# Kernel optimization log

Hardware: AMD Instinct MI355X
Metric: run time of the kernel (lower is better)

Reference implementation:

```python
import jax, jax.numpy as jnp
import numpy as np
import math

H = 128      # hidden_channels
R = 32       # num_rbf
N = 4096     # atoms
E = 65536    # edges
CU = 4.5     # cutoff_upper (cutoff_lower = 0)
ALPHA = 5.0 / CU
MEANS = jnp.linspace(math.exp(-CU), 1.0, R, dtype=jnp.float32)
BETA = jnp.float32((2.0 / R * (1.0 - math.exp(-CU))) ** -2)
EPS = 1e-5


def _ln(x, g, b):
    mu = x.mean(-1, keepdims=True)
    var = ((x - mu) ** 2).mean(-1, keepdims=True)
    return (x - mu) * jax.lax.rsqrt(var + EPS) * g + b


def setup_inputs() -> dict:
    key = jax.random.key(0)
    ks = jax.random.split(key, 20)
    f32 = jnp.float32

    def w(i, shape):
        return jax.random.normal(ks[i], shape, f32) / np.float32(np.sqrt(shape[-1]))

    return {
        "edge_vec": jax.random.normal(ks[0], (E, 3), f32) * 1.5,
        "emb_w": w(1, (128, H)),
        "emb2_w": w(2, (H, 2 * H)), "emb2_b": jnp.zeros((H,), f32),
        "dp1_w": w(3, (H, R)), "dp1_b": jnp.zeros((H,), f32),
        "dp2_w": w(4, (H, R)), "dp2_b": jnp.zeros((H,), f32),
        "dp3_w": w(5, (H, R)), "dp3_b": jnp.zeros((H,), f32),
        "lt0_w": w(6, (H, H)), "lt1_w": w(7, (H, H)), "lt2_w": w(8, (H, H)),
        "ls0_w": w(9, (2 * H, H)), "ls0_b": jnp.zeros((2 * H,), f32),
        "ls1_w": w(10, (3 * H, 2 * H)), "ls1_b": jnp.zeros((3 * H,), f32),
        "init_g": jnp.ones((H,), f32), "init_b": jnp.zeros((H,), f32),
        "lin_w": w(11, (H, 3 * H)), "lin_b": jnp.zeros((H,), f32),
        "outn_g": jnp.ones((3 * H,), f32), "outn_b": jnp.zeros((3 * H,), f32),
        "ol1_w": w(12, (H // 2, H)), "ol1_b": jnp.zeros((H // 2,), f32),
        "ol2_w": w(13, (1, H // 2)), "ol2_b": jnp.zeros((1,), f32),
        "z": jax.random.randint(ks[14], (N,), 0, 128, dtype=jnp.int32),
        "edge_index": jax.random.randint(ks[15], (2, E), 0, N, dtype=jnp.int32),
    }


def reference(edge_vec, emb_w, emb2_w, emb2_b, dp1_w, dp1_b, dp2_w, dp2_b,
              dp3_w, dp3_b, lt0_w, lt1_w, lt2_w, ls0_w, ls0_b, ls1_w, ls1_b,
              init_g, init_b, lin_w, lin_b, outn_g, outn_b, ol1_w, ol1_b,
              ol2_w, ol2_b, z, edge_index):
    n = z.shape[0]
    src, dst = edge_index[0], edge_index[1]

    d = jnp.sqrt((edge_vec ** 2).sum(-1))                 # (E,)
    vn = edge_vec / d[:, None]                             # unit edge vectors
    cut = jnp.where(d < CU, 0.5 * (jnp.cos(jnp.pi * d / CU) + 1.0), 0.0)
    # expnorm RBF
    rbf = cut[:, None] * jnp.exp(-BETA * (jnp.exp(-ALPHA * d)[:, None] - MEANS) ** 2)  # (E,R)

    # atomic-number message Zij = emb2(cat(emb(z_i), emb(z_j)))
    zpair = jnp.concatenate([emb_w[z[src]], emb_w[z[dst]]], -1)  # (E,2H)
    zij = zpair @ emb2_w.T + emb2_b                              # (E,H)
    c = cut[:, None] * zij                                       # cutoff * Zij, (E,H)

    w1 = (rbf @ dp1_w.T + dp1_b) * c    # scalar channel weights (E,H)
    w2 = (rbf @ dp2_w.T + dp2_b) * c
    w3 = (rbf @ dp3_w.T + dp3_b) * c

    eye = jnp.eye(3, dtype=edge_vec.dtype)
    zero = jnp.zeros_like(vn[:, 0])
    skew = jnp.stack([zero, -vn[:, 2], vn[:, 1],
                      vn[:, 2], zero, -vn[:, 0],
                      -vn[:, 1], vn[:, 0], zero], 1).reshape(-1, 3, 3)  # (E,3,3)
    outer = vn[:, :, None] * vn[:, None, :]
    sym = outer - ((vn ** 2).sum(-1) / 3.0)[:, None, None] * eye        # traceless sym (E,3,3)

    seg = lambda a: jax.ops.segment_sum(a, src, num_segments=n)
    I0 = seg(w1)[:, :, None, None] * eye                                # (N,H,3,3)
    A0 = seg(w2[:, :, None, None] * skew[:, None, :, :])                # (N,H,3,3)
    S0 = seg(w3[:, :, None, None] * sym[:, None, :, :])                 # (N,H,3,3)

    tn = ((I0 + A0 + S0) ** 2).sum((-2, -1))                            # tensor_norm, (N,H)
    nrm = _ln(tn, init_g, init_b)
    h = jax.nn.silu(nrm @ ls0_w.T + ls0_b)
    scal = jax.nn.silu(h @ ls1_w.T + ls1_b).reshape(n, H, 3)            # per-channel gates

    I1 = jnp.einsum('nhxy,gh->ngxy', I0, lt0_w) * scal[..., 0][..., None, None]
    A1 = jnp.einsum('nhxy,gh->ngxy', A0, lt1_w) * scal[..., 1][..., None, None]
    S1 = jnp.einsum('nhxy,gh->ngxy', S0, lt2_w) * scal[..., 2][..., None, None]

    x = jnp.concatenate([(I1 ** 2).sum((-2, -1)),
                         (A1 ** 2).sum((-2, -1)),
                         (S1 ** 2).sum((-2, -1))], -1)                  # (N,3H)
    x = _ln(x, outn_g, outn_b)
    s1 = x @ lin_w.T + lin_b
    s2 = jax.nn.silu(s1) @ ol1_w.T + ol1_b
    s3 = jax.nn.silu(s2) @ ol2_w.T + ol2_b                              # per-atom energy (N,1)
    return s3
```

## Files before the change

### kernel.cpp

```cpp
#include <hip/hip_runtime.h>
#include <math.h>

#define NH_TOT 524288
#define N_ATOM 4096
#define N_EDGE 65536

typedef __attribute__((ext_vector_type(8))) short bf16x8;
typedef __attribute__((ext_vector_type(4))) float f32x4;

__device__ __forceinline__ unsigned short f2bf(float f) {
    unsigned u = __builtin_bit_cast(unsigned, f);
    unsigned r = (u + 0x7fffu + ((u >> 16) & 1u)) >> 16;
    return (unsigned short)r;
}
__device__ __forceinline__ float silu(float v) { return v / (1.0f + __expf(-v)); }

#define WB_LS1 32768
#define WB_LT0 131072
#define WB_LT1 147456
#define WB_LT2 163840
#define WB_DP  180224

__global__ __launch_bounds__(256) void k_setup(
    const float* __restrict__ emb_w, const float* __restrict__ emb2_w,
    const int* __restrict__ ei,
    const float* __restrict__ ls0_w, const float* __restrict__ ls1_w,
    const float* __restrict__ lt0_w, const float* __restrict__ lt1_w,
    const float* __restrict__ lt2_w,
    const float* __restrict__ dp1_w, const float* __restrict__ dp2_w,
    const float* __restrict__ dp3_w,
    float* __restrict__ U1, float* __restrict__ U2,
    int* __restrict__ cursor, int* __restrict__ order_pad,
    unsigned short* __restrict__ wb) {
    const int bx = blockIdx.x, tid = threadIdx.x;
    if (bx < 4096) {
        const int idx = bx * 4 + (tid >> 6);
        const int t = idx >> 7, h = idx & 127;
        const int lane = tid & 63;
        const float e0 = emb_w[t * 128 + lane];
        const float e1 = emb_w[t * 128 + 64 + lane];
        const float* row = emb2_w + h * 256;
        const float w0 = row[lane], w1 = row[64 + lane];
        const float w2 = row[128 + lane], w3 = row[192 + lane];
        float u1 = e0 * w0 + e1 * w1;
        float u2 = e0 * w2 + e1 * w3;
#pragma unroll
        for (int o = 1; o < 64; o <<= 1) {
            u1 += __shfl_xor(u1, o, 64);
            u2 += __shfl_xor(u2, o, 64);
        }
        if (lane == 0) {
            U1[t * 128 + h] = u1;
            U2[t * 128 + h] = u2;
        }
    } else if (bx < 4352) {
        const int e = (bx - 4096) * 256 + tid;
        const int src = ei[e];
        const int pos = atomicAdd(&cursor[src], 1);
        if (pos < 64) order_pad[(src << 6) + pos] = e;
    } else {
        const int base = (bx - 4352) * 1024 + tid * 4;
        const float* src;
        int off;
        if (base < 32768)       { src = ls0_w; off = 0; }
        else if (base < 131072) { src = ls1_w; off = 32768; }
        else if (base < 147456) { src = lt0_w; off = 131072; }
        else if (base < 163840) { src = lt1_w; off = 147456; }
        else if (base < 180224) { src = lt2_w; off = 163840; }
        else if (base < 184320) { src = dp1_w; off = 180224; }
        else if (base < 188416) { src = dp2_w; off = 184320; }
        else                    { src = dp3_w; off = 188416; }
        const float4 v = *(const float4*)(src + (base - off));
        unsigned short* o = wb + base;
        o[0] = f2bf(v.x); o[1] = f2bf(v.y); o[2] = f2bf(v.z); o[3] = f2bf(v.w);
    }
}

__global__ __launch_bounds__(256) void k_fused(
    const int* __restrict__ z, const int* __restrict__ ecnt,
    const int* __restrict__ order_pad, const int* __restrict__ ei,
    const float* __restrict__ edge_vec,
    const float* __restrict__ U1, const float* __restrict__ U2,
    const float* __restrict__ emb2_b,
    const float* __restrict__ dp1_b, const float* __restrict__ dp2_b,
    const float* __restrict__ dp3_b,
    const unsigned short* __restrict__ wb,
    const float* __restrict__ init_g, const float* __restrict__ init_b,
    const float* __restrict__ ls0_b, const float* __restrict__ ls1_b,
    const float* __restrict__ outn_g, const float* __restrict__ outn_b,
    const float* __restrict__ lin_w, const float* __restrict__ lin_b,
    const float* __restrict__ ol1_w, const float* __restrict__ ol1_b,
    const float* __restrict__ ol2_w, const float* __restrict__ ol2_b,
    float* __restrict__ out) {
    const int tid = threadIdx.x;
    const int wave = tid >> 6, lane = tid & 63, lm = lane & 15, lq = lane >> 4;
    const int n0 = blockIdx.x * 8;
    const int ar = (lm < 8) ? lm : 7;

    __shared__ alignas(16) unsigned short accs[10][8][136];
    __shared__ alignas(16) unsigned short nrms[8][136];
    __shared__ unsigned short h1[16][280];
    __shared__ float scal_s[8][388];
    __shared__ float ss[8][132];
    __shared__ float redS[8][4];
    __shared__ float redQ[8][4];
    float (*xs)[392] = reinterpret_cast<float(*)[392]>(&accs[0][0][0]);

    const unsigned short* dpw = wb + WB_DP;
    bf16x8 bfr[3][2];
    float bhc[2], bk1[2], bk2[2], bk3[2];
    int cols[2];
#pragma unroll
    for (int t = 0; t < 2; t++) {
        const int col = wave * 32 + t * 16 + lm;
        cols[t] = col;
        bhc[t] = emb2_b[col];
        bk1[t] = dp1_b[col]; bk2[t] = dp2_b[col]; bk3[t] = dp3_b[col];
#pragma unroll
        for (int k = 0; k < 3; k++)
            bfr[k][t] = *(const bf16x8*)(dpw + k * 4096 + col * 32 + lq * 8);
    }

    const float m0 = 0.011108996538242306f;
    const float dm = (1.0f - m0) * (1.0f / 31.0f);
    const float tb = 0.0625f * (1.0f - m0);
    const float beta = 1.0f / (tb * tb);
    const float mean0 = m0 + (float)(lq * 8) * dm;

    float tnA[8], tnB[8];

    for (int nn = 0; nn < 8; nn++) {
        const int n = n0 + nn;
        const int En = min(ecnt[n], 64);
        const int beg = n << 6;
        const int zoff = z[n] << 7;
        const float u1c0 = U1[zoff + cols[0]];
        const float u1c1 = U1[zoff + cols[1]];

        float part[10][2];
#pragma unroll
        for (int p = 0; p < 10; p++) { part[p][0] = 0.f; part[p][1] = 0.f; }

        for (int mi = 0; mi < En; mi += 16) {
            const int e = order_pad[beg + min(mi + lm, En - 1)];
            const float evx = edge_vec[3 * e + 0];
            const float evy = edge_vec[3 * e + 1];
            const float evz = edge_vec[3 * e + 2];
            const float d = sqrtf(evx * evx + evy * evy + evz * evz);
            const float inv = 1.0f / d;
            const float cut = (d < 4.5f) ? 0.5f * (__cosf(0.6981317007977318f * d) + 1.0f) : 0.0f;
            const float vx = evx * inv, vy = evy * inv, vz = evz * inv;
            const int u2o = z[ei[N_EDGE + e]] << 7;
            const float expd = __expf(-1.1111111111111112f * d);

            union { bf16x8 v; unsigned short s[8]; } uf;
#pragma unroll
            for (int j = 0; j < 8; j++) {
                const float df = expd - (mean0 + (float)j * dm);
                uf.s[j] = f2bf(cut * __expf(-beta * df * df));
            }
            const bf16x8 af = uf.v;

            f32x4 c[3][2];
#pragma unroll
            for (int k = 0; k < 3; k++)
#pragma unroll
                for (int t = 0; t < 2; t++)
                    c[k][t] = __builtin_amdgcn_mfma_f32_16x16x32_bf16(
                        af, bfr[k][t], (f32x4){0.f, 0.f, 0.f, 0.f}, 0, 0, 0);

#pragma unroll
            for (int r = 0; r < 4; r++) {
                const int er = mi + lq * 4 + r;
                const bool valid = er < En;
                const int sl = (lane & 48) | (lq * 4 + r);
                const float gvx = __shfl(vx, sl, 64);
                const float gvy = __shfl(vy, sl, 64);
                const float gvz = __shfl(vz, sl, 64);
                const float gct = __shfl(cut, sl, 64);
                const int   go  = __shfl(u2o, sl, 64);
#pragma unroll
                for (int t = 0; t < 2; t++) {
                    const float u2v = U2[go + cols[t]];
                    const float u1h = (t == 0) ? u1c0 : u1c1;
                    const float cc = valid ? gct * (u1h + u2v + bhc[t]) : 0.f;
                    const float w1 = (c[0][t][r] + bk1[t]) * cc;
                    const float w2 = (c[1][t][r] + bk2[t]) * cc;
                    const float w3 = (c[2][t][r] + bk3[t]) * cc;
                    part[0][t] += w1;
                    part[1][t] += w2 * gvx; part[2][t] += w2 * gvy; part[3][t] += w2 * gvz;
                    const float tx = w3 * gvx, ty = w3 * gvy;
                    part[4][t] += tx * gvx; part[5][t] += tx * gvy; part[6][t] += tx * gvz;
                    part[7][t] += ty * gvy; part[8][t] += ty * gvz; part[9][t] += w3 * gvz * gvz;
                }
            }
        }

#pragma unroll
        for (int p = 0; p < 10; p++)
#pragma unroll
            for (int t = 0; t < 2; t++) {
                float v = part[p][t];
                v += __shfl_xor(v, 16, 64);
                v += __shfl_xor(v, 32, 64);
                part[p][t] = v;
            }
        if (lq == 0) {
#pragma unroll
            for (int p = 0; p < 10; p++)
#pragma unroll
                for (int t = 0; t < 2; t++)
                    accs[p][nn][cols[t]] = f2bf(part[p][t]);
        }

        float tn[2];
#pragma unroll
        for (int t = 0; t < 2; t++) {
            const float aI = part[0][t];
            const float axv = part[1][t], ayv = part[2][t], azv = part[3][t];
            const float mxx = part[4][t], mxy = part[5][t], mxz = part[6][t];
            const float myy = part[7][t], myz = part[8][t], mzz = part[9][t];
            const float tr3 = (mxx + myy + mzz) * (1.0f / 3.0f);
            const float t00 = aI + mxx - tr3;
            const float t11 = aI + myy - tr3;
            const float t22 = aI + mzz - tr3;
            tn[t] = t00 * t00 + t11 * t11 + t22 * t22 +
                    2.0f * (mxy * mxy + azv * azv + mxz * mxz + ayv * ayv + myz * myz + axv * axv);
        }
        tnA[nn] = tn[0];
        tnB[nn] = tn[1];

        float s = (lq == 0) ? (tn[0] + tn[1]) : 0.f;
        s += __shfl_xor(s, 1, 64);
        s += __shfl_xor(s, 2, 64);
        s += __shfl_xor(s, 4, 64);
        s += __shfl_xor(s, 8, 64);
        if (lane == 0) redS[nn][wave] = s;
    }
    __syncthreads();

    {
        float dvA[8], dvB[8];
#pragma unroll
        for (int nn = 0; nn < 8; nn++) {
            const float mu = (redS[nn][0] + redS[nn][1] + redS[nn][2] + redS[nn][3]) * (1.0f / 128.0f);
            dvA[nn] = tnA[nn] - mu;
            dvB[nn] = tnB[nn] - mu;
            float q = (lq == 0) ? (dvA[nn] * dvA[nn] + dvB[nn] * dvB[nn]) : 0.f;
            q += __shfl_xor(q, 1, 64);
            q += __shfl_xor(q, 2, 64);
            q += __shfl_xor(q, 4, 64);
            q += __shfl_xor(q, 8, 64);
            if (lane == 0) redQ[nn][wave] = q;
        }
        __syncthreads();
        if (lq == 0) {
            const float g0 = init_g[cols[0]], g1 = init_g[cols[1]];
            const float b0 = init_b[cols[0]], b1 = init_b[cols[1]];
#pragma unroll
            for (int nn = 0; nn < 8; nn++) {
                const float var = (redQ[nn][0] + redQ[nn][1] + redQ[nn][2] + redQ[nn][3]) * (1.0f / 128.0f);
                const float rs = rsqrtf(var + 1e-5f);
                nrms[nn][cols[0]] = f2bf(dvA[nn] * rs * g0 + b0);
                nrms[nn][cols[1]] = f2bf(dvB[nn] * rs * g1 + b1);
            }
        }
    }
    __syncthreads();

    {
        f32x4 acc[4];
#pragma unroll
        for (int j = 0; j < 4; j++) acc[j] = (f32x4){0.f, 0.f, 0.f, 0.f};
        const int cbase = wave * 64;
#pragma unroll
        for (int kc = 0; kc < 128; kc += 32) {
            const bf16x8 af = *(const bf16x8*)(&nrms[ar][kc + lq * 8]);
#pragma unroll
            for (int sn = 0; sn < 4; sn++) {
                const bf16x8 b = *(const bf16x8*)(wb + (size_t)(cbase + sn * 16 + lm) * 128 + kc + lq * 8);
                acc[sn] = __builtin_amdgcn_mfma_f32_16x16x32_bf16(af, b, acc[sn], 0, 0, 0);
            }
        }
#pragma unroll
        for (int sn = 0; sn < 4; sn++) {
            const int col = cbase + sn * 16 + lm;
            const float bv = ls0_b[col];
#pragma unroll
            for (int r = 0; r < 4; r++)
                h1[lq * 4 + r][col] = f2bf(silu(acc[sn][r] + bv));
        }
    }
    __syncthreads();
    {
        f32x4 acc[6];
#pragma unroll
        for (int j = 0; j < 6; j++) acc[j] = (f32x4){0.f, 0.f, 0.f, 0.f};
        const int cbase = wave * 96;
        const unsigned short* ls1p = wb + WB_LS1;
#pragma unroll 2
        for (int kc = 0; kc < 256; kc += 32) {
            const bf16x8 af = *(const bf16x8*)(&h1[lm][kc + lq * 8]);
#pragma unroll
            for (int sn = 0; sn < 6; sn++) {
                const bf16x8 b = *(const bf16x8*)(ls1p + (size_t)(cbase + sn * 16 + lm) * 256 + kc + lq * 8);
                acc[sn] = __builtin_amdgcn_mfma_f32_16x16x32_bf16(af, b, acc[sn], 0, 0, 0);
            }
        }
#pragma unroll
        for (int sn = 0; sn < 6; sn++) {
            const int col = cbase + sn * 16 + lm;
            const float bv = ls1_b[col];
#pragma unroll
            for (int r = 0; r < 4; r++) {
                const int node = lq * 4 + r;
                if (node < 8) scal_s[node][col] = silu(acc[sn][r] + bv);
            }
        }
    }
    __syncthreads();

    f32x4 e0[2], e1[2], e2[2], trv[2];
#pragma unroll
    for (int sn = 0; sn < 2; sn++) {
        e0[sn] = (f32x4){0.f, 0.f, 0.f, 0.f};
        e1[sn] = (f32x4){0.f, 0.f, 0.f, 0.f};
        e2[sn] = (f32x4){0.f, 0.f, 0.f, 0.f};
        trv[sn] = (f32x4){0.f, 0.f, 0.f, 0.f};
    }
#pragma unroll
    for (int p = 0; p < 10; p++) {
        const unsigned short* B = wb + (p == 0 ? WB_LT0 : (p < 4 ? WB_LT1 : WB_LT2));
        f32x4 c[2];
        c[0] = (f32x4){0.f, 0.f, 0.f, 0.f};
        c[1] = (f32x4){0.f, 0.f, 0.f, 0.f};
#pragma unroll
        for (int kc = 0; kc < 128; kc += 32) {
            const bf16x8 af = *(const bf16x8*)(&accs[p][ar][kc + lq * 8]);
#pragma unroll
            for (int sn = 0; sn < 2; sn++) {
                const bf16x8 b = *(const bf16x8*)(B + (size_t)(wave * 32 + sn * 16 + lm) * 128 + kc + lq * 8);
                c[sn] = __builtin_amdgcn_mfma_f32_16x16x32_bf16(af, b, c[sn], 0, 0, 0);
            }
        }
#pragma unroll
        for (int sn = 0; sn < 2; sn++) {
            if (p == 0)      e0[sn] += c[sn] * c[sn];
            else if (p < 4)  e1[sn] += c[sn] * c[sn];
            else if (p == 4 || p == 7 || p == 9) { e2[sn] += c[sn] * c[sn]; trv[sn] += c[sn]; }
            else             e2[sn] += 2.0f * c[sn] * c[sn];
        }
    }
    __syncthreads();

    if (lq < 2) {
#pragma unroll
        for (int sn = 0; sn < 2; sn++) {
            const int g = wave * 32 + sn * 16 + lm;
#pragma unroll
            for (int r = 0; r < 4; r++) {
                const int node = lq * 4 + r;
                const float s0 = scal_s[node][3 * g + 0];
                const float s1 = scal_s[node][3 * g + 1];
                const float s2 = scal_s[node][3 * g + 2];
                xs[node][g]       = 3.0f * e0[sn][r] * s0 * s0;
                xs[node][128 + g] = 2.0f * e1[sn][r] * s1 * s1;
                const float tr = trv[sn][r];
                xs[node][256 + g] = (e2[sn][r] - tr * tr * (1.0f / 3.0f)) * s2 * s2;
            }
        }
    }
    __syncthreads();

#pragma unroll
    for (int i = 0; i < 2; i++) {
        const int node = wave * 2 + i;
        float v[6];
        float s = 0.f;
#pragma unroll
        for (int j = 0; j < 6; j++) { v[j] = xs[node][lane + 64 * j]; s += v[j]; }
#pragma unroll
        for (int o = 1; o < 64; o <<= 1) s += __shfl_xor(s, o, 64);
        const float mu = s * (1.0f / 384.0f);
        float q = 0.f;
#pragma unroll
        for (int j = 0; j < 6; j++) { v[j] -= mu; q += v[j] * v[j]; }
#pragma unroll
        for (int o = 1; o < 64; o <<= 1) q += __shfl_xor(q, o, 64);
        const float rs = rsqrtf(q * (1.0f / 384.0f) + 1e-5f);
#pragma unroll
        for (int j = 0; j < 6; j++) {
            const int col = lane + 64 * j;
            xs[node][col] = v[j] * rs * outn_g[col] + outn_b[col];
        }
    }
    __syncthreads();

    {
        const int j = tid & 127, half = tid >> 7;
        float a4[4];
        const float lb = lin_b[j];
#pragma unroll
        for (int i = 0; i < 4; i++) a4[i] = lb;
        const float4* wr = (const float4*)(lin_w + j * 384);
#pragma unroll 2
        for (int k4 = 0; k4 < 96; k4++) {
            const float4 w4 = wr[k4];
#pragma unroll
            for (int i = 0; i < 4; i++) {
                const float4 xv = *(const float4*)&xs[half * 4 + i][k4 * 4];
                a4[i] += w4.x * xv.x + w4.y * xv.y + w4.z * xv.z + w4.w * xv.w;
            }
        }
#pragma unroll
        for (int i = 0; i < 4; i++) ss[half * 4 + i][j] = silu(a4[i]);
    }
    __syncthreads();

    {
        const int o = tid & 63, q = tid >> 6;
        float a2v[2];
        const float ob = ol1_b[o];
        a2v[0] = ob; a2v[1] = ob;
        const float4* o4 = (const float4*)(ol1_w + o * 128);
#pragma unroll 4
        for (int k4 = 0; k4 < 32; k4++) {
            const float4 w4 = o4[k4];
#pragma unroll
            for (int i = 0; i < 2; i++) {
                const float4 sv = *(const float4*)&ss[q * 2 + i][k4 * 4];
                a2v[i] += w4.x * sv.x + w4.y * sv.y + w4.z * sv.z + w4.w * sv.w;
            }
        }
        const float w2 = ol2_w[o];
#pragma unroll
        for (int i = 0; i < 2; i++) {
            float v = silu(a2v[i]) * w2;
            for (int s = 32; s > 0; s >>= 1) v += __shfl_down(v, s, 64);
            if (o == 0) out[n0 + q * 2 + i] = v + ol2_b[0];
        }
    }
}

extern "C" void kernel_launch(void* const* d_in, const int* in_sizes, int n_in,
                              void* d_out, int out_size, void* d_ws, size_t ws_size,
                              hipStream_t stream) {
    (void)in_sizes; (void)n_in; (void)out_size; (void)ws_size;
    const float* edge_vec = (const float*)d_in[0];
    const float* emb_w   = (const float*)d_in[1];
    const float* emb2_w  = (const float*)d_in[2];
    const float* emb2_b  = (const float*)d_in[3];
    const float* dp1_w   = (const float*)d_in[4];
    const float* dp1_b   = (const float*)d_in[5];
    const float* dp2_w   = (const float*)d_in[6];
    const float* dp2_b   = (const float*)d_in[7];
    const float* dp3_w   = (const float*)d_in[8];
    const float* dp3_b   = (const float*)d_in[9];
    const float* lt0_w   = (const float*)d_in[10];
    const float* lt1_w   = (const float*)d_in[11];
    const float* lt2_w   = (const float*)d_in[12];
    const float* ls0_w   = (const float*)d_in[13];
    const float* ls0_b   = (const float*)d_in[14];
    const float* ls1_w   = (const float*)d_in[15];
    const float* ls1_b   = (const float*)d_in[16];
    const float* init_g  = (const float*)d_in[17];
    const float* init_b  = (const float*)d_in[18];
    const float* lin_w   = (const float*)d_in[19];
    const float* lin_b   = (const float*)d_in[20];
    const float* outn_g  = (const float*)d_in[21];
    const float* outn_b  = (const float*)d_in[22];
    const float* ol1_w   = (const float*)d_in[23];
    const float* ol1_b   = (const float*)d_in[24];
    const float* ol2_w   = (const float*)d_in[25];
    const float* ol2_b   = (const float*)d_in[26];
    const int* z  = (const int*)d_in[27];
    const int* ei = (const int*)d_in[28];
    float* out = (float*)d_out;

    char* w = (char*)d_ws;
    int*            cursor    = (int*)(w);
    unsigned short* wb        = (unsigned short*)(w + 16384);
    float*          U1        = (float*)(w + 401408);
    float*          U2        = (float*)(w + 466944);
    int*            order_pad = (int*)(w + 532480);

    hipMemsetAsync(w, 0, 16384, stream);
    k_setup<<<dim3(4540), dim3(256), 0, stream>>>(emb_w, emb2_w, ei,
                                                  ls0_w, ls1_w, lt0_w, lt1_w, lt2_w,
                                                  dp1_w, dp2_w, dp3_w,
                                                  U1, U2, cursor, order_pad, wb);
    k_fused<<<dim3(512), dim3(256), 0, stream>>>(z, cursor, order_pad, ei, edge_vec,
                                                 U1, U2, emb2_b, dp1_b, dp2_b, dp3_b, wb,
                                                 init_g, init_b, ls0_b, ls1_b,
                                                 outn_g, outn_b, lin_w, lin_b,
                                                 ol1_w, ol1_b, ol2_w, ol2_b, out);
}
```

Baseline: 213.3 us.

## Pack dst atom type into edge order list and shrink shared memory footprint

During the bucketing pass, the destination atom's type is packed into the upper 16 bits of each edge index. This removes the dependent ei-then-z gather from the per-edge loop in the fused kernel. Shared memory is consolidated into one aliased buffer: the per-channel gates are stored as bf16, the h1 padding is reduced, and ss now aliases h1. A launch bound of 4 is added to target higher occupancy. The aliasing requires an extra barrier, bf16 gates lose some precision, and the packing assumes edge ids fit in 16 bits.

New measurement: 237.9 us. 11.5% more time.

```diff
diff --git a/kernel.cpp b/kernel.cpp
--- a/kernel.cpp
+++ b/kernel.cpp
@@ -13,6 +13,10 @@
     unsigned r = (u + 0x7fffu + ((u >> 16) & 1u)) >> 16;
     return (unsigned short)r;
 }
+__device__ __forceinline__ float bf2f(unsigned short s) {
+    unsigned u = ((unsigned)s) << 16;
+    return __builtin_bit_cast(float, u);
+}
 __device__ __forceinline__ float silu(float v) { return v / (1.0f + __expf(-v)); }
 
 #define WB_LS1 32768
@@ -23,7 +27,7 @@
 
 __global__ __launch_bounds__(256) void k_setup(
     const float* __restrict__ emb_w, const float* __restrict__ emb2_w,
-    const int* __restrict__ ei,
+    const int* __restrict__ ei, const int* __restrict__ z,
     const float* __restrict__ ls0_w, const float* __restrict__ ls1_w,
     const float* __restrict__ lt0_w, const float* __restrict__ lt1_w,
     const float* __restrict__ lt2_w,
@@ -56,8 +60,9 @@
     } else if (bx < 4352) {
         const int e = (bx - 4096) * 256 + tid;
         const int src = ei[e];
+        const int zd = z[ei[N_EDGE + e]];
         const int pos = atomicAdd(&cursor[src], 1);
-        if (pos < 64) order_pad[(src << 6) + pos] = e;
+        if (pos < 64) order_pad[(src << 6) + pos] = e | (zd << 16);
     } else {
         const int base = (bx - 4352) * 1024 + tid * 4;
         const float* src;
@@ -76,9 +81,9 @@
     }
 }
 
-__global__ __launch_bounds__(256) void k_fused(
+__global__ __launch_bounds__(256, 4) void k_fused(
     const int* __restrict__ z, const int* __restrict__ ecnt,
-    const int* __restrict__ order_pad, const int* __restrict__ ei,
+    const int* __restrict__ order_pad,
     const float* __restrict__ edge_vec,
     const float* __restrict__ U1, const float* __restrict__ U2,
     const float* __restrict__ emb2_b,
@@ -97,14 +102,15 @@
     const int n0 = blockIdx.x * 8;
     const int ar = (lm < 8) ? lm : 7;
 
-    __shared__ alignas(16) unsigned short accs[10][8][136];
-    __shared__ alignas(16) unsigned short nrms[8][136];
-    __shared__ unsigned short h1[16][280];
-    __shared__ float scal_s[8][388];
-    __shared__ float ss[8][132];
-    __shared__ float redS[8][4];
-    __shared__ float redQ[8][4];
-    float (*xs)[392] = reinterpret_cast<float(*)[392]>(&accs[0][0][0]);
+    __shared__ alignas(16) char smem[38912];
+    unsigned short (*accs)[8][136] = reinterpret_cast<unsigned short(*)[8][136]>(smem);
+    unsigned short (*nrms)[136]    = reinterpret_cast<unsigned short(*)[136]>(smem + 21760);
+    unsigned short (*h1)[264]      = reinterpret_cast<unsigned short(*)[264]>(smem + 23936);
+    unsigned short (*scal_s)[392]  = reinterpret_cast<unsigned short(*)[392]>(smem + 32384);
+    float (*redS)[4]               = reinterpret_cast<float(*)[4]>(smem + 38656);
+    float (*redQ)[4]               = reinterpret_cast<float(*)[4]>(smem + 38784);
+    float (*xs)[392]               = reinterpret_cast<float(*)[392]>(smem);
+    float (*ss)[132]               = reinterpret_cast<float(*)[132]>(smem + 23936);
 
     const unsigned short* dpw = wb + WB_DP;
     bf16x8 bfr[3][2];
@@ -142,7 +148,9 @@
         for (int p = 0; p < 10; p++) { part[p][0] = 0.f; part[p][1] = 0.f; }
 
         for (int mi = 0; mi < En; mi += 16) {
-            const int e = order_pad[beg + min(mi + lm, En - 1)];
+            const int wrd = order_pad[beg + min(mi + lm, En - 1)];
+            const int e = wrd & 0xFFFF;
+            const int u2o = (wrd >> 16) << 7;
             const float evx = edge_vec[3 * e + 0];
             const float evy = edge_vec[3 * e + 1];
             const float evz = edge_vec[3 * e + 2];
@@ -150,7 +158,6 @@
             const float inv = 1.0f / d;
             const float cut = (d < 4.5f) ? 0.5f * (__cosf(0.6981317007977318f * d) + 1.0f) : 0.0f;
             const float vx = evx * inv, vy = evy * inv, vz = evz * inv;
-            const int u2o = z[ei[N_EDGE + e]] << 7;
             const float expd = __expf(-1.1111111111111112f * d);
 
             union { bf16x8 v; unsigned short s[8]; } uf;
@@ -314,7 +321,7 @@
 #pragma unroll
             for (int r = 0; r < 4; r++) {
                 const int node = lq * 4 + r;
-                if (node < 8) scal_s[node][col] = silu(acc[sn][r] + bv);
+                if (node < 8) scal_s[node][col] = f2bf(silu(acc[sn][r] + bv));
             }
         }
     }
@@ -360,9 +367,9 @@
 #pragma unroll
             for (int r = 0; r < 4; r++) {
                 const int node = lq * 4 + r;
-                const float s0 = scal_s[node][3 * g + 0];
-                const float s1 = scal_s[node][3 * g + 1];
-                const float s2 = scal_s[node][3 * g + 2];
+                const float s0 = bf2f(scal_s[node][3 * g + 0]);
+                const float s1 = bf2f(scal_s[node][3 * g + 1]);
+                const float s2 = bf2f(scal_s[node][3 * g + 2]);
                 xs[node][g]       = 3.0f * e0[sn][r] * s0 * s0;
                 xs[node][128 + g] = 2.0f * e1[sn][r] * s1 * s1;
                 const float tr = trv[sn][r];
@@ -412,6 +419,7 @@
                 a4[i] += w4.x * xv.x + w4.y * xv.y + w4.z * xv.z + w4.w * xv.w;
             }
         }
+        __syncthreads();
 #pragma unroll
         for (int i = 0; i < 4; i++) ss[half * 4 + i][j] = silu(a4[i]);
     }
@@ -485,11 +493,11 @@
     int*            order_pad = (int*)(w + 532480);
 
     hipMemsetAsync(w, 0, 16384, stream);
-    k_setup<<<dim3(4540), dim3(256), 0, stream>>>(emb_w, emb2_w, ei,
+    k_setup<<<dim3(4540), dim3(256), 0, stream>>>(emb_w, emb2_w, ei, z,
                                                   ls0_w, ls1_w, lt0_w, lt1_w, lt2_w,
                                                   dp1_w, dp2_w, dp3_w,
                                                   U1, U2, cursor, order_pad, wb);
-    k_fused<<<dim3(512), dim3(256), 0, stream>>>(z, cursor, order_pad, ei, edge_vec,
+    k_fused<<<dim3(512), dim3(256), 0, stream>>>(z, cursor, order_pad, edge_vec,
                                                  U1, U2, emb2_b, dp1_b, dp2_b, dp3_b, wb,
                                                  init_g, init_b, ls0_b, ls1_b,
                                                  outn_g, outn_b, lin_w, lin_b,
```
